# Performance work log

Hardware: AMD Instinct MI355X
Metric: run time of the kernel (lower is better)

## Reference

```python
import jax, jax.numpy as jnp
import numpy as np

B, N, C_IN, C_OUT, BASIS = 8, 128, 64, 64, 15
AVG_NOBJ = 49.0
NEG_SLOPE = 0.01  # torch LeakyReLU default


def eops_2_to_2_sum(x, average_nobj=AVG_NOBJ):
    """x: [B, C, N, N] -> [B, C, 15, N, N].
    5 order-zero ops + 10 sum-aggregation ops (sums normalized by average_nobj,
    double sums by average_nobj**2, as in PELICAN's 'sum' aggregation)."""
    n = x.shape[-1]
    eye = jnp.eye(n, dtype=x.dtype)                       # [N, N]
    d = jnp.diagonal(x, axis1=-2, axis2=-1)               # [B, C, N]
    rowsum = x.sum(-1) / average_nobj                      # [B, C, N]
    colsum = x.sum(-2) / average_nobj                      # [B, C, N]
    trace = d.sum(-1) / average_nobj                       # [B, C]
    allsum = x.sum((-2, -1)) / (average_nobj ** 2)         # [B, C]
    bc = lambda v: jnp.broadcast_to(v, x.shape)
    ops = [
        # --- order zero (no aggregation) ---
        d[..., :, None] * eye,                 # diag(A) embedded on diagonal
        bc(d[..., :, None]),                   # A_ii broadcast along j
        bc(d[..., None, :]),                   # A_jj broadcast along i
        x,                                     # identity
        jnp.swapaxes(x, -1, -2),               # transpose
        # --- aggregation ops ---
        rowsum[..., :, None] * eye,            # row sums on diagonal
        colsum[..., :, None] * eye,            # col sums on diagonal
        trace[..., None, None] * eye,          # trace on diagonal
        allsum[..., None, None] * eye,         # total sum on diagonal
        bc(rowsum[..., :, None]),              # rowsum_i broadcast along j
        bc(rowsum[..., None, :]),              # rowsum_j broadcast along i
        bc(colsum[..., :, None]),              # colsum_i broadcast along j
        bc(colsum[..., None, :]),              # colsum_j broadcast along i
        bc(trace[..., None, None]),            # trace broadcast everywhere
        bc(allsum[..., None, None]),           # total sum broadcast everywhere
    ]
    return jnp.stack(ops, axis=2)              # [B, C, 15, N, N]


def setup_inputs() -> dict:
    key = jax.random.key(0)
    ks = jax.random.split(key, 5)
    inputs = jax.random.normal(ks[0], (B, N, N, C_IN), jnp.float32)
    mask = jnp.ones((B, N, N, 1), jnp.float32)
    nobj = jnp.full((B,), float(N), jnp.float32)
    s_b = float(np.sqrt(1.0 / BASIS))
    s_d = float(np.sqrt(1.0 / C_IN))
    coefs00 = jax.random.normal(ks[1], (C_IN, BASIS), jnp.float32) * s_b
    coefs01 = jax.random.normal(ks[2], (C_OUT, BASIS), jnp.float32) * s_b
    coefs10 = jax.random.normal(ks[3], (C_IN, C_OUT), jnp.float32) * s_d
    coefs11 = jax.random.normal(ks[4], (C_IN, C_OUT), jnp.float32) * s_d
    bias = jnp.zeros((C_OUT,), jnp.float32)
    diag_bias = jnp.zeros((C_OUT,), jnp.float32)
    return {"inputs": inputs, "mask": mask, "nobj": nobj,
            "coefs00": coefs00, "coefs01": coefs01,
            "coefs10": coefs10, "coefs11": coefs11,
            "bias": bias, "diag_bias": diag_bias}


def reference(inputs, mask, nobj, coefs00, coefs01, coefs10, coefs11, bias, diag_bias):
    # inputs: [B, N, N, C_in] -> channels-first for basis construction
    x = jnp.transpose(inputs, (0, 3, 1, 2))                     # [B, C, N, N]
    ops = eops_2_to_2_sum(x)                                    # [B, C, 15, N, N]
    # low-rank reconstructed coefficient tensor [C_in, C_out, 15]
    coefs = (coefs00[:, None, :] * coefs10[:, :, None]
             + coefs01[None, :, :] * coefs11[:, :, None])
    out = jnp.einsum('dsb,ndbij->nijs', coefs, ops)             # [B, N, N, C_out]
    eye = jnp.eye(inputs.shape[1], dtype=out.dtype)[None, :, :, None]
    out = out + bias[None, None, None, :] + eye * diag_bias[None, None, None, :]
    out = jax.nn.leaky_relu(out, NEG_SLOPE)
    return out * mask
```

## Files before the change

kernel.cpp:

```cpp
#include <hip/hip_runtime.h>

#define BB 8
#define NN 128
#define CC 64
static constexpr float INV_A = 1.0f / 49.0f;

#define OFF_C    0
#define OFF_CB   61440
#define OFF_RS   65536
#define OFF_CS   131072
#define OFF_DV   196608
#define OFF_U1   263168
#define OFF_U2   328704
#define OFF_DG   394240

typedef __attribute__((ext_vector_type(8))) short v8s;
typedef __attribute__((ext_vector_type(4))) float v4f;

static __device__ inline unsigned pack2bf(float a, float b) {
    union { float f; unsigned u; } ua, ub; ua.f = a; ub.f = b;
    return ((ua.u + 0x8000u) >> 16) | ((ub.u + 0x8000u) & 0xffff0000u);
}
static __device__ inline unsigned short f2bf(float a) {
    union { float f; unsigned u; } ua; ua.f = a;
    return (unsigned short)((ua.u + 0x8000u) >> 16);
}

__global__ void k_pre(const float* __restrict__ in,
                      const float* __restrict__ c00, const float* __restrict__ c01,
                      const float* __restrict__ c10, const float* __restrict__ c11,
                      float* __restrict__ ws) {
    if (blockIdx.x >= 512) {
        int idx = (blockIdx.x - 512) * 256 + threadIdx.x;
        if (idx < 15 * 4096) {
            int b = idx >> 12; int r = idx & 4095; int d = r >> 6; int s = r & 63;
            ws[OFF_C + idx] = c00[d * 15 + b] * c10[d * 64 + s] + c01[s * 15 + b] * c11[d * 64 + s];
        } else if (idx < 15 * 4096 + 8192) {
            int k = idx - 15 * 4096;
            int which = k >> 12;
            int r = k & 4095; int s = r >> 6; int d = r & 63;
            int b = 3 + which;
            float v = c00[d * 15 + b] * c10[d * 64 + s] + c01[s * 15 + b] * c11[d * 64 + s];
            unsigned short* cb = (unsigned short*)(ws + OFF_CB);
            cb[s * 128 + which * 64 + d] = f2bf(v);
        }
        return;
    }
    __shared__ float4 part[4][4][16];
    int mode = blockIdx.x >> 8;
    int bb = blockIdx.x & 255;
    int n = bb >> 5; int g0 = (bb & 31) * 4;
    int t = threadIdx.x;
    int q = t >> 6; int ii = (t >> 4) & 3; int d4 = t & 15;
    float4 acc = make_float4(0.f, 0.f, 0.f, 0.f);
    if (mode == 0) {
        int i = g0 + ii;
        float4 dvv = acc; bool hd = false;
        const float* base = in + ((size_t)(n * NN + i)) * NN * CC + d4 * 4;
        for (int j = q * 32; j < q * 32 + 32; ++j) {
            float4 v = *(const float4*)(base + (size_t)j * CC);
            acc.x += v.x; acc.y += v.y; acc.z += v.z; acc.w += v.w;
            if (j == i) { dvv = v; hd = true; }
        }
        if (hd) *(float4*)(ws + OFF_DV + ((size_t)(n * NN + i)) * CC + d4 * 4) = dvv;
    } else {
        int j = g0 + ii;
        for (int i = q * 32; i < q * 32 + 32; ++i) {
            float4 v = *(const float4*)(in + (((size_t)(n * NN + i)) * NN + j) * CC + d4 * 4);
            acc.x += v.x; acc.y += v.y; acc.z += v.z; acc.w += v.w;
        }
    }
    part[q][ii][d4] = acc;
    __syncthreads();
    if (t < 64) {
        int i2 = t >> 4; int dd = t & 15;
        float4 a = part[0][i2][dd], b = part[1][i2][dd], c = part[2][i2][dd], d = part[3][i2][dd];
        float4 s;
        s.x = (a.x + b.x + c.x + d.x) * INV_A;
        s.y = (a.y + b.y + c.y + d.y) * INV_A;
        s.z = (a.z + b.z + c.z + d.z) * INV_A;
        s.w = (a.w + b.w + c.w + d.w) * INV_A;
        *(float4*)(ws + (mode ? OFF_CS : OFF_RS) + ((size_t)(n * NN + g0 + i2)) * CC + dd * 4) = s;
    }
}

__global__ __launch_bounds__(256, 4) void k_uv(const float* __restrict__ bias,
                                               const float* __restrict__ dbias,
                                               float* __restrict__ ws) {
    __shared__ float trL[64], asL[64];
    __shared__ float pU1[4][4][64], pU2[4][4][64], pDG[4][4][64];
    __shared__ float pS[4][64], pDGc[4][64];
    int n = blockIdx.x >> 5; int i0 = (blockIdx.x & 31) * 4;
    int t = threadIdx.x;
    int s = t & 63; int q = t >> 6;

    {
        float tr = 0.f, as = 0.f;
        #pragma unroll 4
        for (int e = 0; e < 32; ++e) {
            int i = q * 32 + e;
            tr += ws[OFF_DV + ((size_t)(n * NN + i)) * CC + s];
            as += ws[OFF_RS + ((size_t)(n * NN + i)) * CC + s];
        }
        pS[q][s] = tr; pDGc[q][s] = as;
        __syncthreads();
        if (t < 64) {
            trL[t] = (pS[0][t] + pS[1][t] + pS[2][t] + pS[3][t]) * INV_A;
            asL[t] = (pDGc[0][t] + pDGc[1][t] + pDGc[2][t] + pDGc[3][t]) * INV_A;
        }
        __syncthreads();
    }

    const float* C = ws + OFF_C;
    float aU1[4] = {0, 0, 0, 0}, aU2[4] = {0, 0, 0, 0}, aDG[4] = {0, 0, 0, 0};
    float aS = 0.f, aDGc = 0.f;
    #pragma unroll
    for (int c4 = 0; c4 < 4; ++c4) {
        int dc = q * 4 + c4;
        float tr4[4], as4[4], dv4[4][4], rs4[4][4], cs4[4][4];
        #pragma unroll
        for (int k = 0; k < 4; ++k) { tr4[k] = trL[dc * 4 + k]; as4[k] = asL[dc * 4 + k]; }
        #pragma unroll
        for (int ii = 0; ii < 4; ++ii) {
            size_t ro = ((size_t)(n * NN + i0 + ii)) * CC + dc * 4;
            float4 v = *(const float4*)(ws + OFF_DV + ro);
            dv4[ii][0] = v.x; dv4[ii][1] = v.y; dv4[ii][2] = v.z; dv4[ii][3] = v.w;
            float4 r = *(const float4*)(ws + OFF_RS + ro);
            rs4[ii][0] = r.x; rs4[ii][1] = r.y; rs4[ii][2] = r.z; rs4[ii][3] = r.w;
            float4 c = *(const float4*)(ws + OFF_CS + ro);
            cs4[ii][0] = c.x; cs4[ii][1] = c.y; cs4[ii][2] = c.z; cs4[ii][3] = c.w;
        }
        #pragma unroll
        for (int k = 0; k < 4; ++k) {
            int d = dc * 4 + k;
            const float* Cd = C + d * 64 + s;
            float c0 = Cd[0 * 4096], c1 = Cd[1 * 4096], c2 = Cd[2 * 4096];
            float c5 = Cd[5 * 4096], c6 = Cd[6 * 4096], c7 = Cd[7 * 4096];
            float c8 = Cd[8 * 4096], c9 = Cd[9 * 4096], c10v = Cd[10 * 4096];
            float c11v = Cd[11 * 4096], c12v = Cd[12 * 4096];
            float c13 = Cd[13 * 4096], c14 = Cd[14 * 4096];
            aS += c13 * tr4[k] + c14 * as4[k];
            aDGc += c7 * tr4[k] + c8 * as4[k];
            #pragma unroll
            for (int ii = 0; ii < 4; ++ii) {
                aU1[ii] += c1 * dv4[ii][k] + c9 * rs4[ii][k] + c11v * cs4[ii][k];
                aU2[ii] += c2 * dv4[ii][k] + c10v * rs4[ii][k] + c12v * cs4[ii][k];
                aDG[ii] += c0 * dv4[ii][k] + c5 * rs4[ii][k] + c6 * cs4[ii][k];
            }
        }
    }
    #pragma unroll
    for (int ii = 0; ii < 4; ++ii) {
        pU1[q][ii][s] = aU1[ii]; pU2[q][ii][s] = aU2[ii]; pDG[q][ii][s] = aDG[ii];
    }
    pS[q][s] = aS; pDGc[q][s] = aDGc;
    __syncthreads();

    int fi = q;
    float u1 = pU1[0][fi][s] + pU1[1][fi][s] + pU1[2][fi][s] + pU1[3][fi][s];
    float u2 = pU2[0][fi][s] + pU2[1][fi][s] + pU2[2][fi][s] + pU2[3][fi][s];
    float dg = pDG[0][fi][s] + pDG[1][fi][s] + pDG[2][fi][s] + pDG[3][fi][s];
    float aSt = pS[0][s] + pS[1][s] + pS[2][s] + pS[3][s];
    float aDGct = pDGc[0][s] + pDGc[1][s] + pDGc[2][s] + pDGc[3][s];
    size_t row = ((size_t)(n * NN + i0 + fi)) * CC + s;
    ws[OFF_U1 + row] = u1 + aSt + bias[s];
    ws[OFF_U2 + row] = u2;
    ws[OFF_DG + row] = dg + aDGct + dbias[s];
}

__global__ __launch_bounds__(256, 4) void k_main(
        const float* __restrict__ in, const float* __restrict__ mask,
        const float* __restrict__ ws, float* __restrict__ out) {
    __shared__ __align__(16) unsigned char smem[34816];
    unsigned short* Ab = (unsigned short*)smem;
    unsigned short* Bb = (unsigned short*)(smem + 17408);
    float* Obuf = (float*)smem;

    int blk = blockIdx.x;
    int n = blk >> 8; int rem = blk & 255; int i = rem >> 1; int j0 = (rem & 1) * 64;
    int t = threadIdx.x;
    int tp = t >> 4; int c = t & 15;

    const unsigned short* cb = (const unsigned short*)(ws + OFF_CB);
    #pragma unroll
    for (int e = 0; e < 4; ++e) {
        int s = e * 16 + tp;
        float4 v = *(const float4*)(cb + s * 128 + c * 8);
        *(float4*)((unsigned char*)(Bb + s * 136 + c * 8)) = v;
    }
    {
        const float* src = in + (((size_t)(n * NN + i)) * NN + j0) * CC;
        #pragma unroll
        for (int e = 0; e < 4; ++e) {
            int p = e * 16 + tp;
            float4 v = *(const float4*)(src + (size_t)p * CC + c * 4);
            uint2 pk; pk.x = pack2bf(v.x, v.y); pk.y = pack2bf(v.z, v.w);
            *(uint2*)(Ab + p * 136 + c * 4) = pk;
        }
    }
    #pragma unroll
    for (int e = 0; e < 4; ++e) {
        int p = e * 16 + tp;
        const float* src = in + (((size_t)(n * NN + (j0 + p))) * NN + i) * CC;
        float4 v = *(const float4*)(src + c * 4);
        uint2 pk; pk.x = pack2bf(v.x, v.y); pk.y = pack2bf(v.z, v.w);
        *(uint2*)(Ab + p * 136 + 64 + c * 4) = pk;
    }
    __syncthreads();

    int w = t >> 6; int l = t & 63;
    int r16 = l & 15; int quad = l >> 4;
    v4f acc[4];
    #pragma unroll
    for (int st = 0; st < 4; ++st) acc[st] = 0.f;
    int arow = w * 16 + r16;
    #pragma unroll
    for (int kk = 0; kk < 4; ++kk) {
        v8s af = *(const v8s*)(Ab + arow * 136 + kk * 32 + quad * 8);
        #pragma unroll
        for (int st = 0; st < 4; ++st) {
            v8s bfr = *(const v8s*)(Bb + (st * 16 + r16) * 136 + kk * 32 + quad * 8);
            acc[st] = __builtin_amdgcn_mfma_f32_16x16x32_bf16(af, bfr, acc[st], 0, 0, 0);
        }
    }
    #pragma unroll
    for (int st = 0; st < 4; ++st)
        #pragma unroll
        for (int reg = 0; reg < 4; ++reg)
            Obuf[(w * 16 + quad * 4 + reg) * 68 + st * 16 + r16] = acc[st][reg];
    __syncthreads();

    int srow = (n * NN + i) * CC;
    float4 u1 = *(const float4*)(ws + OFF_U1 + srow + c * 4);
    float4 dg = *(const float4*)(ws + OFF_DG + srow + c * 4);
    #pragma unroll
    for (int e = 0; e < 4; ++e) {
        int p = e * 16 + tp;
        int j = j0 + p;
        float4 v = *(const float4*)(Obuf + p * 68 + c * 4);
        float4 u2 = *(const float4*)(ws + OFF_U2 + (n * NN + j) * CC + c * 4);
        v.x += u1.x + u2.x; v.y += u1.y + u2.y; v.z += u1.z + u2.z; v.w += u1.w + u2.w;
        if (j == i) { v.x += dg.x; v.y += dg.y; v.z += dg.z; v.w += dg.w; }
        v.x = v.x > 0.f ? v.x : 0.01f * v.x;
        v.y = v.y > 0.f ? v.y : 0.01f * v.y;
        v.z = v.z > 0.f ? v.z : 0.01f * v.z;
        v.w = v.w > 0.f ? v.w : 0.01f * v.w;
        float m = mask[((size_t)(n * NN + i)) * NN + j];
        v.x *= m; v.y *= m; v.z *= m; v.w *= m;
        *(float4*)(out + (((size_t)(n * NN + i)) * NN + j) * CC + c * 4) = v;
    }
}

extern "C" void kernel_launch(void* const* d_in, const int* in_sizes, int n_in,
                              void* d_out, int out_size, void* d_ws, size_t ws_size,
                              hipStream_t stream) {
    const float* inputs = (const float*)d_in[0];
    const float* mask   = (const float*)d_in[1];
    const float* c00 = (const float*)d_in[3];
    const float* c01 = (const float*)d_in[4];
    const float* c10 = (const float*)d_in[5];
    const float* c11 = (const float*)d_in[6];
    const float* bias  = (const float*)d_in[7];
    const float* dbias = (const float*)d_in[8];
    float* out = (float*)d_out;
    float* ws = (float*)d_ws;

    k_pre <<<784, 256, 0, stream>>>(inputs, c00, c01, c10, c11, ws);
    k_uv  <<<256, 256, 0, stream>>>(bias, dbias, ws);
    k_main<<<2048, 256, 0, stream>>>(inputs, mask, ws, out);
}
```

Baseline: 136.9 us.

## Tile main kernel over symmetric 8x8 block pairs and pre-convert input to bf16

k_pre now writes a bf16 copy of the full input into workspace while computing row sums. k_main tiles the (i,j) plane into 8x8 blocks and processes only upper-triangular block pairs (I<=J). Each block loads the x[i,j] and x[j,i] halves once and computes both the (I,J) and (J,I) output tiles by swapping the K-halves of the A fragments, which halves the input reads. The cost is an extra bf16 write pass in k_pre, fewer blocks (1088 instead of 2048), and a second epilogue pass with more registers per thread.

New measurement: 139.0 us. About the same (+1.5%).

```diff
diff --git a/kernel.cpp b/kernel.cpp
--- a/kernel.cpp
+++ b/kernel.cpp
@@ -3,6 +3,7 @@
 #define BB 8
 #define NN 128
 #define CC 64
+#define NT 16
 static constexpr float INV_A = 1.0f / 49.0f;
 
 #define OFF_C    0
@@ -13,6 +14,7 @@
 #define OFF_U1   263168
 #define OFF_U2   328704
 #define OFF_DG   394240
+#define OFF_XB   459776
 
 typedef __attribute__((ext_vector_type(8))) short v8s;
 typedef __attribute__((ext_vector_type(4))) float v4f;
@@ -57,9 +59,13 @@
         int i = g0 + ii;
         float4 dvv = acc; bool hd = false;
         const float* base = in + ((size_t)(n * NN + i)) * NN * CC + d4 * 4;
+        unsigned short* xB = (unsigned short*)(ws + OFF_XB)
+                           + ((size_t)(n * NN + i)) * NN * CC + d4 * 4;
         for (int j = q * 32; j < q * 32 + 32; ++j) {
             float4 v = *(const float4*)(base + (size_t)j * CC);
             acc.x += v.x; acc.y += v.y; acc.z += v.z; acc.w += v.w;
+            uint2 pk; pk.x = pack2bf(v.x, v.y); pk.y = pack2bf(v.z, v.w);
+            *(uint2*)(xB + (size_t)j * CC) = pk;
             if (j == i) { dvv = v; hd = true; }
         }
         if (hd) *(float4*)(ws + OFF_DV + ((size_t)(n * NN + i)) * CC + d4 * 4) = dvv;
@@ -169,7 +175,7 @@
 }
 
 __global__ __launch_bounds__(256, 4) void k_main(
-        const float* __restrict__ in, const float* __restrict__ mask,
+        const float* __restrict__ mask,
         const float* __restrict__ ws, float* __restrict__ out) {
     __shared__ __align__(16) unsigned char smem[34816];
     unsigned short* Ab = (unsigned short*)smem;
@@ -177,7 +183,11 @@
     float* Obuf = (float*)smem;
 
     int blk = blockIdx.x;
-    int n = blk >> 8; int rem = blk & 255; int i = rem >> 1; int j0 = (rem & 1) * 64;
+    int n = blk / 136; int rem = blk - n * 136;
+    int I = 0;
+    { int rr = rem; while (rr >= NT - I) { rr -= NT - I; ++I; } rem = rr; }
+    int J = I + rem;
+    int i0 = I * 8, j0 = J * 8;
     int t = threadIdx.x;
     int tp = t >> 4; int c = t & 15;
 
@@ -188,66 +198,92 @@
         float4 v = *(const float4*)(cb + s * 128 + c * 8);
         *(float4*)((unsigned char*)(Bb + s * 136 + c * 8)) = v;
     }
-    {
-        const float* src = in + (((size_t)(n * NN + i)) * NN + j0) * CC;
-        #pragma unroll
-        for (int e = 0; e < 4; ++e) {
-            int p = e * 16 + tp;
-            float4 v = *(const float4*)(src + (size_t)p * CC + c * 4);
-            uint2 pk; pk.x = pack2bf(v.x, v.y); pk.y = pack2bf(v.z, v.w);
-            *(uint2*)(Ab + p * 136 + c * 4) = pk;
-        }
-    }
+    const unsigned short* xb = (const unsigned short*)(ws + OFF_XB);
+    #pragma unroll
+    for (int e = 0; e < 4; ++e) {
+        int idx = e * 256 + t;
+        int chunk = idx & 7; int row = idx >> 3;
+        int hh = row >> 6; int p = row & 63;
+        int ii = p >> 3, jj = p & 7;
+        int gi = hh ? (j0 + jj) : (i0 + ii);
+        int gj = hh ? (i0 + ii) : (j0 + jj);
+        float4 v = *(const float4*)(xb + (((size_t)(n * NN + gi)) * NN + gj) * CC + chunk * 8);
+        *(float4*)((unsigned char*)(Ab + p * 136 + hh * 64 + chunk * 8)) = v;
+    }
+    __syncthreads();
+
+    int w = t >> 6; int l = t & 63;
+    int r16 = l & 15; int quad = l >> 4;
+    int arow = w * 16 + r16;
+    v8s af[4];
+    #pragma unroll
+    for (int kk = 0; kk < 4; ++kk)
+        af[kk] = *(const v8s*)(Ab + arow * 136 + kk * 32 + quad * 8);
+    v4f acc1[4], acc2[4];
+    #pragma unroll
+    for (int st = 0; st < 4; ++st) { acc1[st] = 0.f; acc2[st] = 0.f; }
+    #pragma unroll
+    for (int kk = 0; kk < 4; ++kk) {
+        #pragma unroll
+        for (int st = 0; st < 4; ++st) {
+            v8s bfr = *(const v8s*)(Bb + (st * 16 + r16) * 136 + kk * 32 + quad * 8);
+            acc1[st] = __builtin_amdgcn_mfma_f32_16x16x32_bf16(af[kk], bfr, acc1[st], 0, 0, 0);
+            acc2[st] = __builtin_amdgcn_mfma_f32_16x16x32_bf16(af[(kk + 2) & 3], bfr, acc2[st], 0, 0, 0);
+        }
+    }
+
+    #pragma unroll
+    for (int st = 0; st < 4; ++st)
+        #pragma unroll
+        for (int reg = 0; reg < 4; ++reg)
+            Obuf[(w * 16 + quad * 4 + reg) * 68 + st * 16 + r16] = acc1[st][reg];
+    __syncthreads();
     #pragma unroll
     for (int e = 0; e < 4; ++e) {
         int p = e * 16 + tp;
-        const float* src = in + (((size_t)(n * NN + (j0 + p))) * NN + i) * CC;
-        float4 v = *(const float4*)(src + c * 4);
-        uint2 pk; pk.x = pack2bf(v.x, v.y); pk.y = pack2bf(v.z, v.w);
-        *(uint2*)(Ab + p * 136 + 64 + c * 4) = pk;
-    }
-    __syncthreads();
-
-    int w = t >> 6; int l = t & 63;
-    int r16 = l & 15; int quad = l >> 4;
-    v4f acc[4];
-    #pragma unroll
-    for (int st = 0; st < 4; ++st) acc[st] = 0.f;
-    int arow = w * 16 + r16;
-    #pragma unroll
-    for (int kk = 0; kk < 4; ++kk) {
-        v8s af = *(const v8s*)(Ab + arow * 136 + kk * 32 + quad * 8);
-        #pragma unroll
-        for (int st = 0; st < 4; ++st) {
-            v8s bfr = *(const v8s*)(Bb + (st * 16 + r16) * 136 + kk * 32 + quad * 8);
-            acc[st] = __builtin_amdgcn_mfma_f32_16x16x32_bf16(af, bfr, acc[st], 0, 0, 0);
-        }
-    }
-    #pragma unroll
-    for (int st = 0; st < 4; ++st)
-        #pragma unroll
-        for (int reg = 0; reg < 4; ++reg)
-            Obuf[(w * 16 + quad * 4 + reg) * 68 + st * 16 + r16] = acc[st][reg];
-    __syncthreads();
-
-    int srow = (n * NN + i) * CC;
-    float4 u1 = *(const float4*)(ws + OFF_U1 + srow + c * 4);
-    float4 dg = *(const float4*)(ws + OFF_DG + srow + c * 4);
-    #pragma unroll
-    for (int e = 0; e < 4; ++e) {
-        int p = e * 16 + tp;
-        int j = j0 + p;
+        int gi = i0 + (p >> 3), gj = j0 + (p & 7);
+        size_t prow = ((size_t)(n * NN + gi));
         float4 v = *(const float4*)(Obuf + p * 68 + c * 4);
-        float4 u2 = *(const float4*)(ws + OFF_U2 + (n * NN + j) * CC + c * 4);
+        float4 u1 = *(const float4*)(ws + OFF_U1 + prow * CC + c * 4);
+        float4 u2 = *(const float4*)(ws + OFF_U2 + ((size_t)(n * NN + gj)) * CC + c * 4);
         v.x += u1.x + u2.x; v.y += u1.y + u2.y; v.z += u1.z + u2.z; v.w += u1.w + u2.w;
-        if (j == i) { v.x += dg.x; v.y += dg.y; v.z += dg.z; v.w += dg.w; }
+        if (gi == gj) {
+            float4 dg = *(const float4*)(ws + OFF_DG + prow * CC + c * 4);
+            v.x += dg.x; v.y += dg.y; v.z += dg.z; v.w += dg.w;
+        }
         v.x = v.x > 0.f ? v.x : 0.01f * v.x;
         v.y = v.y > 0.f ? v.y : 0.01f * v.y;
         v.z = v.z > 0.f ? v.z : 0.01f * v.z;
         v.w = v.w > 0.f ? v.w : 0.01f * v.w;
-        float m = mask[((size_t)(n * NN + i)) * NN + j];
+        float m = mask[prow * NN + gj];
         v.x *= m; v.y *= m; v.z *= m; v.w *= m;
-        *(float4*)(out + (((size_t)(n * NN + i)) * NN + j) * CC + c * 4) = v;
+        *(float4*)(out + (prow * NN + gj) * CC + c * 4) = v;
+    }
+
+    if (I == J) return;
+    __syncthreads();
+    #pragma unroll
+    for (int st = 0; st < 4; ++st)
+        #pragma unroll
+        for (int reg = 0; reg < 4; ++reg)
+            Obuf[(w * 16 + quad * 4 + reg) * 68 + st * 16 + r16] = acc2[st][reg];
+    __syncthreads();
+    #pragma unroll
+    for (int e = 0; e < 4; ++e) {
+        int p = e * 16 + tp;
+        int gi = j0 + (p & 7), gj = i0 + (p >> 3);
+        size_t prow = ((size_t)(n * NN + gi));
+        float4 v = *(const float4*)(Obuf + p * 68 + c * 4);
+        float4 u1 = *(const float4*)(ws + OFF_U1 + prow * CC + c * 4);
+        float4 u2 = *(const float4*)(ws + OFF_U2 + ((size_t)(n * NN + gj)) * CC + c * 4);
+        v.x += u1.x + u2.x; v.y += u1.y + u2.y; v.z += u1.z + u2.z; v.w += u1.w + u2.w;
+        v.x = v.x > 0.f ? v.x : 0.01f * v.x;
+        v.y = v.y > 0.f ? v.y : 0.01f * v.y;
+        v.z = v.z > 0.f ? v.z : 0.01f * v.z;
+        v.w = v.w > 0.f ? v.w : 0.01f * v.w;
+        float m = mask[prow * NN + gj];
+        v.x *= m; v.y *= m; v.z *= m; v.w *= m;
+        *(float4*)(out + (prow * NN + gj) * CC + c * 4) = v;
     }
 }
 
@@ -267,5 +303,5 @@
 
     k_pre <<<784, 256, 0, stream>>>(inputs, c00, c01, c10, c11, ws);
     k_uv  <<<256, 256, 0, stream>>>(bias, dbias, ws);
-    k_main<<<2048, 256, 0, stream>>>(inputs, mask, ws, out);
-}
+    k_main<<<8 * 136, 256, 0, stream>>>(mask, ws, out);
+}
```
